# Kernel optimization log

Measured on AMD Instinct MI355X. Metric: run time of the kernel, lower is better.

The kernel has to match this reference:

```python
import jax, jax.numpy as jnp
import numpy as np

EPS_BN = 1e-3  # nn.BatchNorm1d(num_channels, eps=0.001)
B, C, N = 16, 256, 2048
NUM_SA = 4


def _bn(x, g, b, m, v):
    # eval-mode BatchNorm1d over channel dim of [B, C, N]
    return g[:, None] * (x - m[:, None]) * jax.lax.rsqrt(v[:, None] + EPS_BN) + b[:, None]


def _sa_layer(x, qk_w, v_w, v_b, t_w, t_b, g, b, m, var):
    # q_conv and k_conv share weights -> energy = (Wx)^T (Wx)
    q = jnp.einsum('oc,bcn->bon', qk_w, x)              # [B, C//4, N]
    energy = jnp.einsum('bcm,bcn->bmn', q, q)           # [B, N, N]
    attn = jax.nn.softmax(energy, axis=-1)
    # offset-attention: extra column-sum normalization (dim=1)
    attn = attn / (1e-9 + attn.sum(axis=1, keepdims=True))
    xv = jnp.einsum('oc,bcn->bon', v_w, x) + v_b[:, None]   # [B, C, N]
    x_r = jnp.einsum('bcn,bnm->bcm', xv, attn)              # bmm(x_v, attention)
    t = jnp.einsum('oc,bcn->bon', t_w, x - x_r) + t_b[:, None]
    return x + jax.nn.relu(_bn(t, g, b, m, var))


def setup_inputs() -> dict:
    key = jax.random.key(0)
    ks = jax.random.split(key, 24)
    f32 = jnp.float32
    d = {}
    d['x'] = jax.random.normal(ks[0], (B, C, N), dtype=f32)
    d['conv1_w'] = jax.random.normal(ks[1], (C, C), dtype=f32) * 0.05
    d['conv2_w'] = jax.random.normal(ks[2], (C, C), dtype=f32) * 0.05
    for i, nm in enumerate(['bn1', 'bn2']):
        kk = jax.random.split(ks[3 + i], 4)
        d[nm + '_g'] = 1.0 + 0.05 * jax.random.normal(kk[0], (C,), dtype=f32)
        d[nm + '_b'] = 0.05 * jax.random.normal(kk[1], (C,), dtype=f32)
        d[nm + '_m'] = 0.05 * jax.random.normal(kk[2], (C,), dtype=f32)
        d[nm + '_v'] = jax.random.uniform(kk[3], (C,), dtype=f32, minval=0.5, maxval=1.5)
    d['sa_qk_w'] = jax.random.normal(ks[5], (NUM_SA, C // 4, C), dtype=f32) * 0.05
    d['sa_v_w'] = jax.random.normal(ks[6], (NUM_SA, C, C), dtype=f32) * 0.05
    d['sa_v_b'] = jax.random.normal(ks[7], (NUM_SA, C), dtype=f32) * 0.05
    d['sa_t_w'] = jax.random.normal(ks[8], (NUM_SA, C, C), dtype=f32) * 0.05
    d['sa_t_b'] = jax.random.normal(ks[9], (NUM_SA, C), dtype=f32) * 0.05
    d['sa_g'] = 1.0 + 0.05 * jax.random.normal(ks[10], (NUM_SA, C), dtype=f32)
    d['sa_b'] = 0.05 * jax.random.normal(ks[11], (NUM_SA, C), dtype=f32)
    d['sa_m'] = 0.05 * jax.random.normal(ks[12], (NUM_SA, C), dtype=f32)
    d['sa_var'] = jax.random.uniform(ks[13], (NUM_SA, C), dtype=f32, minval=0.5, maxval=1.5)
    d['flag'] = 0  # False -> primary bn branch
    return d


def reference(x, conv1_w, conv2_w, bn1_g, bn1_b, bn1_m, bn1_v,
              bn2_g, bn2_b, bn2_m, bn2_v,
              sa_qk_w, sa_v_w, sa_v_b, sa_t_w, sa_t_b,
              sa_g, sa_b, sa_m, sa_var, flag):
    h = jax.nn.relu(_bn(jnp.einsum('oc,bcn->bon', conv1_w, x), bn1_g, bn1_b, bn1_m, bn1_v))
    h = jax.nn.relu(_bn(jnp.einsum('oc,bcn->bon', conv2_w, h), bn2_g, bn2_b, bn2_m, bn2_v))
    outs = []
    for i in range(NUM_SA):
        h = _sa_layer(h, sa_qk_w[i], sa_v_w[i], sa_v_b[i], sa_t_w[i], sa_t_b[i],
                      sa_g[i], sa_b[i], sa_m[i], sa_var[i])
        outs.append(h)
    return jnp.concatenate(outs, axis=1)  # [B, 4*C, N]
```

## Files before the change

kernel.cpp:

```cpp
#include <hip/hip_runtime.h>
#include <hip/hip_bf16.h>
#include <hip/hip_fp16.h>

static constexpr int Bn = 16;
static constexpr int Cc = 256;
static constexpr int Nn = 2048;
static constexpr int C4 = 64;
static constexpr float LOG2E = 1.4426950408889634f;

typedef _Float16 half_t;
typedef __attribute__((ext_vector_type(8))) _Float16 half8;
typedef __attribute__((ext_vector_type(4))) _Float16 half4;
typedef __attribute__((ext_vector_type(8))) short short8;
typedef __attribute__((ext_vector_type(4))) float float4v;

static constexpr long sNC = (long)Nn * Cc;
static constexpr long sNQ = (long)Nn * C4;

#define DEVI __device__ __forceinline__

DEVI float bf2f(unsigned short u) { return __uint_as_float(((unsigned)u) << 16); }
DEVI unsigned short f2bf(float f) {
    unsigned x = __float_as_uint(f);
    x += 0x7fffu + ((x >> 16) & 1u);
    return (unsigned short)(x >> 16);
}

DEVI void gload16(const void* g, void* l) {
    __builtin_amdgcn_global_load_lds(
        (const __attribute__((address_space(1))) unsigned int*)g,
        (__attribute__((address_space(3))) unsigned int*)l, 16, 0, 0);
}

enum { EPI_RAW = 0, EPI_H = 1, EPI_XV = 2, EPI_T = 4 };

template<int MODE, int BM, int BN, int WI, int WJ, bool BF16OUT>
__global__ __launch_bounds__(WI * WJ * 64)
void mgemm(const half_t* __restrict__ A, long aB,
           const half_t* __restrict__ Bm, long bB,
           void* __restrict__ Yv, long yB, int ldy,
           const half_t* __restrict__ Haux, long hB,
           half_t* __restrict__ hNext, long hnB,
           const float* __restrict__ bias,
           const float* __restrict__ bng, const float* __restrict__ bnb,
           const float* __restrict__ bnm, const float* __restrict__ bnv,
           int K)
{
    constexpr int NW = WI * WJ;
    __shared__ __align__(16) half_t Als[2][BM][32];
    __shared__ __align__(16) half_t Bls[2][BN][32];

    const int tid  = threadIdx.x;
    const int w    = tid >> 6;
    const int lane = tid & 63;
    const int wi   = w % WI;
    const int wj   = w / WI;
    const int quad = lane >> 4, m16 = lane & 15;
    const int lr   = lane >> 2, lc = lane & 3;
    const int b    = blockIdx.z;
    const int j0   = blockIdx.x * BN;
    const int i0   = blockIdx.y * BM;

    const half_t* Ab = A + (size_t)b * aB;
    const half_t* Bb = Bm + (size_t)b * bB;

    float4v acc[4][4];
    #pragma unroll
    for (int i = 0; i < 4; ++i)
        #pragma unroll
        for (int j = 0; j < 4; ++j) acc[i][j] = (float4v)0.f;

    for (int k0 = 0; k0 < K; k0 += 64) {
        #pragma unroll
        for (int s = 0; s < 2; ++s) {
            const int kk = k0 + s * 32 + lc * 8;
            #pragma unroll
            for (int t = 0; t < BM / (16 * NW); ++t) {
                const int row = (t * NW + w) * 16;
                gload16(Ab + (size_t)(i0 + row + lr) * K + kk, &Als[s][row][0]);
            }
            #pragma unroll
            for (int t = 0; t < BN / (16 * NW); ++t) {
                const int row = (t * NW + w) * 16;
                gload16(Bb + (size_t)(j0 + row + lr) * K + kk, &Bls[s][row][0]);
            }
        }
        __syncthreads();
        #pragma unroll
        for (int s = 0; s < 2; ++s) {
            half8 af[4], bf[4];
            #pragma unroll
            for (int t = 0; t < 4; ++t)
                af[t] = *(const half8*)&Als[s][wi * 64 + t * 16 + m16][quad * 8];
            #pragma unroll
            for (int t = 0; t < 4; ++t)
                bf[t] = *(const half8*)&Bls[s][wj * 64 + t * 16 + m16][quad * 8];
            #pragma unroll
            for (int ti = 0; ti < 4; ++ti)
                #pragma unroll
                for (int tj = 0; tj < 4; ++tj)
                    acc[ti][tj] = __builtin_amdgcn_mfma_f32_16x16x32_f16(
                        af[ti], bf[tj], acc[ti][tj], 0, 0, 0);
        }
        __syncthreads();
    }

    #pragma unroll
    for (int ti = 0; ti < 4; ++ti) {
        const int il = i0 + wi * 64 + ti * 16 + quad * 4;
        #pragma unroll
        for (int tj = 0; tj < 4; ++tj) {
            const int jl = j0 + wj * 64 + tj * 16 + m16;
            float4v v = acc[ti][tj];
            if (MODE == EPI_RAW) {
                half4 o;
                #pragma unroll
                for (int r = 0; r < 4; ++r) o[r] = (half_t)v[r];
                *(half4*)((half_t*)Yv + (size_t)b * yB + (size_t)jl * ldy + il) = o;
            } else if (MODE == EPI_H) {
                half4 o;
                #pragma unroll
                for (int r = 0; r < 4; ++r) {
                    const float sc = bng[il + r] * rsqrtf(bnv[il + r] + 1e-3f);
                    const float sh = bnb[il + r] - bnm[il + r] * sc;
                    o[r] = (half_t)fmaxf(fmaf(v[r], sc, sh), 0.f);
                }
                *(half4*)((half_t*)Yv + (size_t)b * yB + (size_t)jl * ldy + il) = o;
            } else if (MODE == EPI_XV) {
                const float bj = bias[jl];
                if (BF16OUT) {
                    ushort4 o;
                    o.x = f2bf(v[0] + bj); o.y = f2bf(v[1] + bj);
                    o.z = f2bf(v[2] + bj); o.w = f2bf(v[3] + bj);
                    *(ushort4*)((unsigned short*)Yv + (size_t)b * yB + (size_t)jl * ldy + il) = o;
                } else {
                    half4 o;
                    #pragma unroll
                    for (int r = 0; r < 4; ++r) o[r] = (half_t)(v[r] + bj);
                    *(half4*)((half_t*)Yv + (size_t)b * yB + (size_t)jl * ldy + il) = o;
                }
            } else {
                const float tb2 = bias[jl];
                const float sc  = bng[jl] * rsqrtf(bnv[jl] + 1e-3f);
                const float sh  = bnb[jl] - bnm[jl] * sc;
                float4v o;
                #pragma unroll
                for (int r = 0; r < 4; ++r) {
                    const float t2  = v[r] + tb2;
                    const float rel = fmaxf(fmaf(t2, sc, sh), 0.f);
                    const float hv  = (float)Haux[(size_t)b * hB + (size_t)(il + r) * Cc + jl];
                    const float ov  = hv + rel;
                    o[r] = ov;
                    if (hNext)
                        hNext[(size_t)b * hnB + (size_t)(il + r) * Cc + jl] = (half_t)ov;
                }
                *(float4v*)((float*)Yv + (size_t)b * yB + (size_t)jl * ldy + il) = o;
            }
        }
    }
}

__global__ __launch_bounds__(256)
void estats(const half_t* __restrict__ q, float* __restrict__ Pbuf)
{
    __shared__ __align__(16) half_t sA[128 * 64];
    __shared__ __align__(16) half_t sB[128 * 64];
    __shared__ float red[2][2][4][16][2];
    const int tid = threadIdx.x, w = tid >> 6, lane = tid & 63;
    const int wi = w & 1, wj = w >> 1, quad = lane >> 4, m16 = lane & 15;
    const int b = blockIdx.z, j0 = blockIdx.x * 128, i0 = blockIdx.y * 128;
    const half_t* qb = q + (size_t)b * sNQ;

    #pragma unroll
    for (int t = 0; t < 4; ++t) {
        const int g = w * 256 + t * 64 + lane;
        const int r = g >> 3, c = g & 7;
        const int cs = c ^ (r & 7);
        gload16(qb + (size_t)(i0 + r) * 64 + cs * 8, sA + (w * 256 + t * 64) * 8);
        gload16(qb + (size_t)(j0 + r) * 64 + cs * 8, sB + (w * 256 + t * 64) * 8);
    }
    __syncthreads();

    half8 an[4][2], bm[4][2];
    #pragma unroll
    for (int t = 0; t < 4; ++t)
        #pragma unroll
        for (int ks = 0; ks < 2; ++ks) {
            const int pc = ((ks * 4 + quad) ^ (m16 & 7)) * 8;
            an[t][ks] = *(const half8*)&sA[(wi * 64 + t * 16 + m16) * 64 + pc];
            bm[t][ks] = *(const half8*)&sB[(wj * 64 + t * 16 + m16) * 64 + pc];
        }

    #pragma unroll
    for (int tj = 0; tj < 4; ++tj) {
        float4v e[4];
        #pragma unroll
        for (int ti = 0; ti < 4; ++ti) {
            e[ti] = (float4v)0.f;
            e[ti] = __builtin_amdgcn_mfma_f32_16x16x32_f16(an[ti][0], bm[tj][0], e[ti], 0, 0, 0);
            e[ti] = __builtin_amdgcn_mfma_f32_16x16x32_f16(an[ti][1], bm[tj][1], e[ti], 0, 0, 0);
        }
        float lmax = -1e30f;
        #pragma unroll
        for (int ti = 0; ti < 4; ++ti)
            #pragma unroll
            for (int r = 0; r < 4; ++r) lmax = fmaxf(lmax, e[ti][r]);
        lmax = fmaxf(lmax, __shfl_xor(lmax, 16));
        lmax = fmaxf(lmax, __shfl_xor(lmax, 32));
        float ls = 0.f;
        #pragma unroll
        for (int ti = 0; ti < 4; ++ti)
            #pragma unroll
            for (int r = 0; r < 4; ++r) ls += __expf(e[ti][r] - lmax);
        ls += __shfl_xor(ls, 16);
        ls += __shfl_xor(ls, 32);
        if (quad == 0) { red[wi][wj][tj][m16][0] = lmax; red[wi][wj][tj][m16][1] = ls; }
    }
    __syncthreads();
    if (tid < 128) {
        const int wj2 = tid >> 6, tj2 = (tid >> 4) & 3, mm = tid & 15;
        const float m0 = red[0][wj2][tj2][mm][0], s0 = red[0][wj2][tj2][mm][1];
        const float m1 = red[1][wj2][tj2][mm][0], s1 = red[1][wj2][tj2][mm][1];
        const float M = fmaxf(m0, m1);
        const float S = s0 * __expf(m0 - M) + s1 * __expf(m1 - M);
        const int m = j0 + wj2 * 64 + tj2 * 16 + mm;
        *(float2*)(Pbuf + (((size_t)b * Nn + m) * 16 + blockIdx.y) * 2) = make_float2(M, S);
    }
}

__global__ __launch_bounds__(256)
void statsreduce(const float* __restrict__ Pbuf, float* __restrict__ off)
{
    const int id = blockIdx.x * 256 + threadIdx.x;
    const int b = id >> 11, m = id & 2047;
    const float2* p = (const float2*)(Pbuf + ((size_t)b * Nn + m) * 32);
    float M = -1e30f;
    #pragma unroll
    for (int i = 0; i < 16; ++i) M = fmaxf(M, p[i].x);
    float S = 0.f;
    #pragma unroll
    for (int i = 0; i < 16; ++i) S += p[i].y * __expf(p[i].x - M);
    off[(size_t)b * Nn + m] = fmaf(M, LOG2E, __log2f(S));
}

__global__ __launch_bounds__(1024, 4)
void flashxr(const half_t* __restrict__ q, const half_t* __restrict__ xv,
             const half_t* __restrict__ h, const float* __restrict__ off,
             half_t* __restrict__ dS)
{
    __shared__ __align__(16) half_t sQ[128 * 64];
    __shared__ __align__(16) half_t sXV[256 * 128];
    __shared__ __align__(16) half_t sP[128 * 128];

    const int tid = threadIdx.x, w = tid >> 6, lane = tid & 63;
    const int quad = lane >> 4, m16 = lane & 15;
    const int wiE = w & 1, wjE = w >> 1;
    const int wi = w & 3, wj = w >> 2;
    const int b = blockIdx.z, j0 = blockIdx.x * 128;
    const half_t* qb  = q + (size_t)b * sNQ;
    const half_t* xvb = xv + (size_t)b * sNC;

    const int sr = tid >> 3, sc = tid & 7;
    const int qsw = (sc ^ (sr & 7)) * 8;

    gload16(qb + (size_t)(j0 + sr) * 64 + qsw, sP + (size_t)tid * 8);
    gload16(qb + (size_t)sr * 64 + qsw,        sQ + (size_t)tid * 8);
    __syncthreads();
    half8 bq[2];
    #pragma unroll
    for (int ks = 0; ks < 2; ++ks)
        bq[ks] = *(const half8*)&sP[(wjE * 16 + m16) * 64
                                    + (((ks * 4 + quad) ^ (m16 & 7)) * 8)];
    __syncthreads();

    float4v acc[4][2];
    #pragma unroll
    for (int i = 0; i < 4; ++i)
        #pragma unroll
        for (int j = 0; j < 2; ++j) acc[i][j] = (float4v)0.f;
    float csa = 0.f;

    const float* offb = off + (size_t)b * Nn;

    for (int nc = 0; nc < 16; ++nc) {
        #pragma unroll
        for (int t = 0; t < 4; ++t) {
            const int g = t * 1024 + tid;
            const int r = g >> 4, c = g & 15;
            gload16(xvb + (size_t)r * Nn + nc * 128 + ((c ^ (r & 15)) * 8),
                    sXV + (size_t)g * 8);
        }
        __syncthreads();

        const int nbase = nc * 128 + wiE * 64 + quad * 4;
        #pragma unroll
        for (int ti = 0; ti < 4; ++ti) {
            const int arow = (wiE * 64 + ti * 16 + m16) * 64;
            const half8 an0 = *(const half8*)&sQ[arow + ((quad ^ (m16 & 7)) * 8)];
            const half8 an1 = *(const half8*)&sQ[arow + (((4 + quad) ^ (m16 & 7)) * 8)];
            float4v e = (float4v)0.f;
            e = __builtin_amdgcn_mfma_f32_16x16x32_f16(an0, bq[0], e, 0, 0, 0);
            e = __builtin_amdgcn_mfma_f32_16x16x32_f16(an1, bq[1], e, 0, 0, 0);
            const float4v o4 = *(const float4v*)&offb[nbase + ti * 16];
            float c0 = 0.f; ushort4 pk;
            #pragma unroll
            for (int r = 0; r < 4; ++r) {
                const float p = __builtin_amdgcn_exp2f(fmaf(e[r], LOG2E, -o4[r]));
                c0 += p; (&pk.x)[r] = f2bf(p);
            }
            csa += c0;
            const int pc  = wiE * 8 + ti * 2 + (quad >> 1);
            const int sub = (quad & 1) * 4;
            const int mrow = wjE * 16 + m16;
            *(ushort4*)&((unsigned short*)sP)[(size_t)mrow * 128 + (pc ^ m16) * 8 + sub] = pk;
        }
        __syncthreads();

        if (nc < 15)
            gload16(qb + (size_t)((nc + 1) * 128 + sr) * 64 + qsw,
                    sQ + (size_t)tid * 8);

        #pragma unroll
        for (int ks = 0; ks < 4; ++ks) {
            short8 xa[4], pb[2];
            #pragma unroll
            for (int ti = 0; ti < 4; ++ti)
                xa[ti] = *(const short8*)&sXV[(wi * 64 + ti * 16 + m16) * 128
                                              + (((ks * 4 + quad) ^ m16) * 8)];
            #pragma unroll
            for (int tj = 0; tj < 2; ++tj)
                pb[tj] = *(const short8*)&sP[(wj * 32 + tj * 16 + m16) * 128
                                             + (((ks * 4 + quad) ^ m16) * 8)];
            #pragma unroll
            for (int ti = 0; ti < 4; ++ti)
                #pragma unroll
                for (int tj = 0; tj < 2; ++tj)
                    acc[ti][tj] = __builtin_amdgcn_mfma_f32_16x16x32_bf16(
                        xa[ti], pb[tj], acc[ti][tj], 0, 0, 0);
        }
        __syncthreads();
    }

    csa += __shfl_xor(csa, 16);
    csa += __shfl_xor(csa, 32);
    float* fb = (float*)sP;
    if (lane < 16) fb[wiE * 128 + wjE * 16 + lane] = csa;
    __syncthreads();
    float csr[2];
    #pragma unroll
    for (int tj = 0; tj < 2; ++tj) {
        const int m = wj * 32 + tj * 16 + m16;
        csr[tj] = 1.0f / (1e-9f + fb[m] + fb[128 + m]);
    }

    const half_t* hb = h + (size_t)b * sNC;
    half_t* db = dS + (size_t)b * sNC;
    #pragma unroll
    for (int ti = 0; ti < 4; ++ti) {
        const int cg = wi * 64 + ti * 16 + quad * 4;
        #pragma unroll
        for (int tj = 0; tj < 2; ++tj) {
            const int mg = j0 + wj * 32 + tj * 16 + m16;
            const half4 hv = *(const half4*)&hb[(size_t)mg * Cc + cg];
            half4 o;
            #pragma unroll
            for (int r = 0; r < 4; ++r)
                o[r] = (half_t)((float)hv[r] - acc[ti][tj][r] * csr[tj]);
            *(half4*)&db[(size_t)mg * Cc + cg] = o;
        }
    }
}

__global__ __launch_bounds__(256)
void xpose_cast(const float* __restrict__ x, half_t* __restrict__ xT)
{
    __shared__ half_t tile[32][33];
    const int tx = threadIdx.x & 31, ty = threadIdx.x >> 5;
    const int n0 = blockIdx.x * 32, c0 = blockIdx.y * 32, b = blockIdx.z;
    #pragma unroll
    for (int r = 0; r < 4; ++r)
        tile[ty * 4 + r][tx] =
            (half_t)x[((size_t)b * Cc + c0 + ty * 4 + r) * Nn + n0 + tx];
    __syncthreads();
    #pragma unroll
    for (int r = 0; r < 4; ++r)
        xT[((size_t)b * Nn + n0 + ty * 4 + r) * Cc + c0 + tx] = tile[tx][ty * 4 + r];
}

__global__ __launch_bounds__(256)
void castall(const float* __restrict__ c1, const float* __restrict__ c2,
             const float* __restrict__ qk, const float* __restrict__ vw,
             const float* __restrict__ tw, half_t* __restrict__ dst)
{
    const int i = (blockIdx.x * 256 + threadIdx.x) * 4;
    const float* s; int o;
    if      (i < 65536)  { s = c1; o = 0; }
    else if (i < 131072) { s = c2; o = 65536; }
    else if (i < 196608) { s = qk; o = 131072; }
    else if (i < 458752) { s = vw; o = 196608; }
    else                 { s = tw; o = 458752; }
    const float4v v = *(const float4v*)(s + (i - o));
    half4 out;
    #pragma unroll
    for (int r = 0; r < 4; ++r) out[r] = (half_t)v[r];
    *(half4*)(dst + i) = out;
}

extern "C" void kernel_launch(void* const* d_in, const int* in_sizes, int n_in,
                              void* d_out, int out_size, void* d_ws, size_t ws_size,
                              hipStream_t stream)
{
    const float* x    = (const float*)d_in[0];
    const float* c1w  = (const float*)d_in[1];
    const float* c2w  = (const float*)d_in[2];
    const float* bn1g = (const float*)d_in[3], *bn1b = (const float*)d_in[4];
    const float* bn1m = (const float*)d_in[5], *bn1v = (const float*)d_in[6];
    const float* bn2g = (const float*)d_in[7], *bn2b = (const float*)d_in[8];
    const float* bn2m = (const float*)d_in[9], *bn2v = (const float*)d_in[10];
    const float* qkw  = (const float*)d_in[11];
    const float* vw   = (const float*)d_in[12];
    const float* vb   = (const float*)d_in[13];
    const float* tw   = (const float*)d_in[14];
    const float* tb   = (const float*)d_in[15];
    const float* sag  = (const float*)d_in[16];
    const float* sab  = (const float*)d_in[17];
    const float* sam  = (const float*)d_in[18];
    const float* sav  = (const float*)d_in[19];
    float* out = (float*)d_out;

    char* ws = (char*)d_ws;
    const size_t HSZ = (size_t)Bn * Nn * Cc * 2;
    half_t* xT   = (half_t*)(ws);
    half_t* hA   = (half_t*)(ws + HSZ);
    half_t* hBuf = (half_t*)(ws + 2 * HSZ);
    half_t* q_s  = (half_t*)(ws + 3 * HSZ);
    half_t* xv_s = (half_t*)(ws + 3 * HSZ + (size_t)4194304);
    half_t* d_s  = (half_t*)(ws + 4 * HSZ + (size_t)4194304);
    float*  offp = (float*) (ws + 5 * HSZ + (size_t)4194304);
    float*  Pbuf = (float*) (ws + 5 * HSZ + (size_t)4325376);
    half_t* warena = (half_t*)(ws + 5 * HSZ + (size_t)8519680);
    half_t* wc1  = warena;
    half_t* wc2  = wc1 + 65536;
    half_t* wqk  = wc2 + 65536;
    half_t* wv   = wqk + 65536;
    half_t* wt   = wv  + 262144;

    dim3 blk(256);

    castall<<<768, blk, 0, stream>>>(c1w, c2w, qkw, vw, tw, warena);
    xpose_cast<<<dim3(Nn / 32, Cc / 32, Bn), blk, 0, stream>>>(x, xT);

    mgemm<EPI_H, 256, 128, 4, 2, false><<<dim3(16, 1, Bn), dim3(512), 0, stream>>>(
        wc1, 0, xT, sNC, hA, sNC, Cc, nullptr, 0, nullptr, 0,
        nullptr, bn1g, bn1b, bn1m, bn1v, Cc);
    mgemm<EPI_H, 256, 128, 4, 2, false><<<dim3(16, 1, Bn), dim3(512), 0, stream>>>(
        wc2, 0, hA, sNC, hBuf, sNC, Cc, nullptr, 0, nullptr, 0,
        nullptr, bn2g, bn2b, bn2m, bn2v, Cc);

    half_t* hcur = hBuf;
    half_t* hnxt = hA;
    for (int L = 0; L < 4; ++L) {
        mgemm<EPI_RAW, 64, 256, 1, 4, false><<<dim3(8, 1, Bn), blk, 0, stream>>>(
            wqk + (long)L * C4 * Cc, 0, hcur, sNC, q_s, sNQ, C4,
            nullptr, 0, nullptr, 0,
            nullptr, nullptr, nullptr, nullptr, nullptr, Cc);
        estats<<<dim3(16, 16, Bn), blk, 0, stream>>>(q_s, Pbuf);
        statsreduce<<<128, blk, 0, stream>>>(Pbuf, offp);
        mgemm<EPI_XV, 128, 256, 2, 4, true><<<dim3(1, 16, Bn), dim3(512), 0, stream>>>(
            hcur, sNC, wv + (long)L * Cc * Cc, 0, xv_s, (long)Cc * Nn, Nn,
            nullptr, 0, nullptr, 0,
            vb + L * Cc, nullptr, nullptr, nullptr, nullptr, Cc);
        flashxr<<<dim3(16, 1, Bn), dim3(1024), 0, stream>>>(
            q_s, xv_s, hcur, offp, d_s);
        mgemm<EPI_T, 128, 256, 2, 4, false><<<dim3(1, 16, Bn), dim3(512), 0, stream>>>(
            d_s, sNC, wt + (long)L * Cc * Cc, 0,
            out + (long)L * Cc * Nn, (long)4 * Cc * Nn, Nn,
            hcur, sNC, (L < 3) ? hnxt : nullptr, sNC,
            tb + L * Cc, sag + L * Cc, sab + L * Cc, sam + L * Cc, sav + L * Cc,
            Cc);
        half_t* tmp = hcur; hcur = hnxt; hnxt = tmp;
    }
}
```

Baseline: 795.7 us.

## Fuse stats reduction and output transform GEMM into flash attention kernel

The softmax-stats reduction moves into the flashxr prologue, computing per-column offsets into shared memory instead of running a separate statsreduce kernel. The trans-conv GEMM with its BN/ReLU/residual epilogue is fused into flashxr's tail: the x - x_r tile is staged in LDS and multiplied by tw read directly from global. This removes two launches per layer and the round trip of the d_s intermediate through memory. The q tile is also double-buffered so the next tile's load is issued before the energy compute. The cost is more LDS per block (sOff plus a second sQ buffer) and dropping the occupancy hint in launch_bounds. Each block also reads the whole Pbuf slice and the full tw matrix redundantly, and the epilogue does scattered stores to hNext.

```diff
diff --git a/kernel.cpp b/kernel.cpp
--- a/kernel.cpp
+++ b/kernel.cpp
@@ -32,15 +32,13 @@
         (__attribute__((address_space(3))) unsigned int*)l, 16, 0, 0);
 }
 
-enum { EPI_RAW = 0, EPI_H = 1, EPI_XV = 2, EPI_T = 4 };
+enum { EPI_RAW = 0, EPI_H = 1, EPI_XV = 2 };
 
 template<int MODE, int BM, int BN, int WI, int WJ, bool BF16OUT>
 __global__ __launch_bounds__(WI * WJ * 64)
 void mgemm(const half_t* __restrict__ A, long aB,
            const half_t* __restrict__ Bm, long bB,
            void* __restrict__ Yv, long yB, int ldy,
-           const half_t* __restrict__ Haux, long hB,
-           half_t* __restrict__ hNext, long hnB,
            const float* __restrict__ bias,
            const float* __restrict__ bng, const float* __restrict__ bnb,
            const float* __restrict__ bnm, const float* __restrict__ bnv,
@@ -126,7 +124,7 @@
                     o[r] = (half_t)fmaxf(fmaf(v[r], sc, sh), 0.f);
                 }
                 *(half4*)((half_t*)Yv + (size_t)b * yB + (size_t)jl * ldy + il) = o;
-            } else if (MODE == EPI_XV) {
+            } else {
                 const float bj = bias[jl];
                 if (BF16OUT) {
                     ushort4 o;
@@ -139,22 +137,6 @@
                     for (int r = 0; r < 4; ++r) o[r] = (half_t)(v[r] + bj);
                     *(half4*)((half_t*)Yv + (size_t)b * yB + (size_t)jl * ldy + il) = o;
                 }
-            } else {
-                const float tb2 = bias[jl];
-                const float sc  = bng[jl] * rsqrtf(bnv[jl] + 1e-3f);
-                const float sh  = bnb[jl] - bnm[jl] * sc;
-                float4v o;
-                #pragma unroll
-                for (int r = 0; r < 4; ++r) {
-                    const float t2  = v[r] + tb2;
-                    const float rel = fmaxf(fmaf(t2, sc, sh), 0.f);
-                    const float hv  = (float)Haux[(size_t)b * hB + (size_t)(il + r) * Cc + jl];
-                    const float ov  = hv + rel;
-                    o[r] = ov;
-                    if (hNext)
-                        hNext[(size_t)b * hnB + (size_t)(il + r) * Cc + jl] = (half_t)ov;
-                }
-                *(float4v*)((float*)Yv + (size_t)b * yB + (size_t)jl * ldy + il) = o;
             }
         }
     }
@@ -228,34 +210,24 @@
     }
 }
 
-__global__ __launch_bounds__(256)
-void statsreduce(const float* __restrict__ Pbuf, float* __restrict__ off)
+__global__ __launch_bounds__(1024)
+void flashxr(const half_t* __restrict__ q, const half_t* __restrict__ xv,
+             const half_t* __restrict__ h, const float* __restrict__ Pbuf,
+             const half_t* __restrict__ tw, const float* __restrict__ tb,
+             const float* __restrict__ bng, const float* __restrict__ bnb,
+             const float* __restrict__ bnm, const float* __restrict__ bnv,
+             float* __restrict__ outL, half_t* __restrict__ hNext)
 {
-    const int id = blockIdx.x * 256 + threadIdx.x;
-    const int b = id >> 11, m = id & 2047;
-    const float2* p = (const float2*)(Pbuf + ((size_t)b * Nn + m) * 32);
-    float M = -1e30f;
-    #pragma unroll
-    for (int i = 0; i < 16; ++i) M = fmaxf(M, p[i].x);
-    float S = 0.f;
-    #pragma unroll
-    for (int i = 0; i < 16; ++i) S += p[i].y * __expf(p[i].x - M);
-    off[(size_t)b * Nn + m] = fmaf(M, LOG2E, __log2f(S));
-}
-
-__global__ __launch_bounds__(1024, 4)
-void flashxr(const half_t* __restrict__ q, const half_t* __restrict__ xv,
-             const half_t* __restrict__ h, const float* __restrict__ off,
-             half_t* __restrict__ dS)
-{
-    __shared__ __align__(16) half_t sQ[128 * 64];
+    __shared__ __align__(16) half_t sQ[2][128 * 64];
     __shared__ __align__(16) half_t sXV[256 * 128];
     __shared__ __align__(16) half_t sP[128 * 128];
+    __shared__ float sOff[Nn];
 
     const int tid = threadIdx.x, w = tid >> 6, lane = tid & 63;
     const int quad = lane >> 4, m16 = lane & 15;
     const int wiE = w & 1, wjE = w >> 1;
     const int wi = w & 3, wj = w >> 2;
+    const int wiT = w & 1, wjT = w >> 1;
     const int b = blockIdx.z, j0 = blockIdx.x * 128;
     const half_t* qb  = q + (size_t)b * sNQ;
     const half_t* xvb = xv + (size_t)b * sNC;
@@ -264,7 +236,27 @@
     const int qsw = (sc ^ (sr & 7)) * 8;
 
     gload16(qb + (size_t)(j0 + sr) * 64 + qsw, sP + (size_t)tid * 8);
-    gload16(qb + (size_t)sr * 64 + qsw,        sQ + (size_t)tid * 8);
+    gload16(qb + (size_t)sr * 64 + qsw,        &sQ[0][(size_t)tid * 8]);
+
+    {
+        const float* pB = Pbuf + (size_t)b * Nn * 32;
+        for (int i = tid; i < Nn; i += 1024) {
+            const float4v* p4 = (const float4v*)(pB + (size_t)i * 32);
+            float4v v[8];
+            #pragma unroll
+            for (int t = 0; t < 8; ++t) v[t] = p4[t];
+            float M = -1e30f;
+            #pragma unroll
+            for (int t = 0; t < 8; ++t) { M = fmaxf(M, v[t][0]); M = fmaxf(M, v[t][2]); }
+            float S = 0.f;
+            #pragma unroll
+            for (int t = 0; t < 8; ++t) {
+                S += v[t][1] * __expf(v[t][0] - M);
+                S += v[t][3] * __expf(v[t][2] - M);
+            }
+            sOff[i] = fmaf(M, LOG2E, __log2f(S));
+        }
+    }
     __syncthreads();
     half8 bq[2];
     #pragma unroll
@@ -280,9 +272,8 @@
         for (int j = 0; j < 2; ++j) acc[i][j] = (float4v)0.f;
     float csa = 0.f;
 
-    const float* offb = off + (size_t)b * Nn;
-
     for (int nc = 0; nc < 16; ++nc) {
+        const int cur = nc & 1;
         #pragma unroll
         for (int t = 0; t < 4; ++t) {
             const int g = t * 1024 + tid;
@@ -290,18 +281,20 @@
             gload16(xvb + (size_t)r * Nn + nc * 128 + ((c ^ (r & 15)) * 8),
                     sXV + (size_t)g * 8);
         }
-        __syncthreads();
+        if (nc < 15)
+            gload16(qb + (size_t)((nc + 1) * 128 + sr) * 64 + qsw,
+                    &sQ[cur ^ 1][(size_t)tid * 8]);
 
         const int nbase = nc * 128 + wiE * 64 + quad * 4;
         #pragma unroll
         for (int ti = 0; ti < 4; ++ti) {
             const int arow = (wiE * 64 + ti * 16 + m16) * 64;
-            const half8 an0 = *(const half8*)&sQ[arow + ((quad ^ (m16 & 7)) * 8)];
-            const half8 an1 = *(const half8*)&sQ[arow + (((4 + quad) ^ (m16 & 7)) * 8)];
+            const half8 an0 = *(const half8*)&sQ[cur][arow + ((quad ^ (m16 & 7)) * 8)];
+            const half8 an1 = *(const half8*)&sQ[cur][arow + (((4 + quad) ^ (m16 & 7)) * 8)];
             float4v e = (float4v)0.f;
             e = __builtin_amdgcn_mfma_f32_16x16x32_f16(an0, bq[0], e, 0, 0, 0);
             e = __builtin_amdgcn_mfma_f32_16x16x32_f16(an1, bq[1], e, 0, 0, 0);
-            const float4v o4 = *(const float4v*)&offb[nbase + ti * 16];
+            const float4v o4 = *(const float4v*)&sOff[nbase + ti * 16];
             float c0 = 0.f; ushort4 pk;
             #pragma unroll
             for (int r = 0; r < 4; ++r) {
@@ -316,10 +309,6 @@
         }
         __syncthreads();
 
-        if (nc < 15)
-            gload16(qb + (size_t)((nc + 1) * 128 + sr) * 64 + qsw,
-                    sQ + (size_t)tid * 8);
-
         #pragma unroll
         for (int ks = 0; ks < 4; ++ks) {
             short8 xa[4], pb[2];
@@ -354,19 +343,73 @@
     }
 
     const half_t* hb = h + (size_t)b * sNC;
-    half_t* db = dS + (size_t)b * sNC;
+    half_t* sD = sXV;
     #pragma unroll
     for (int ti = 0; ti < 4; ++ti) {
         const int cg = wi * 64 + ti * 16 + quad * 4;
+        const int cc = (cg >> 3) ^ (m16 & 7);
+        const int sub = (quad & 1) * 4;
         #pragma unroll
         for (int tj = 0; tj < 2; ++tj) {
-            const int mg = j0 + wj * 32 + tj * 16 + m16;
+            const int mr = wj * 32 + tj * 16 + m16;
+            const int mg = j0 + mr;
             const half4 hv = *(const half4*)&hb[(size_t)mg * Cc + cg];
             half4 o;
             #pragma unroll
             for (int r = 0; r < 4; ++r)
                 o[r] = (half_t)((float)hv[r] - acc[ti][tj][r] * csr[tj]);
-            *(half4*)&db[(size_t)mg * Cc + cg] = o;
+            *(half4*)&sD[(size_t)mr * 256 + cc * 8 + sub] = o;
+        }
+    }
+    __syncthreads();
+
+    float4v acc2[4][2];
+    #pragma unroll
+    for (int i = 0; i < 4; ++i)
+        #pragma unroll
+        for (int j = 0; j < 2; ++j) acc2[i][j] = (float4v)0.f;
+    #pragma unroll
+    for (int ks = 0; ks < 8; ++ks) {
+        half8 af[4], bf[2];
+        #pragma unroll
+        for (int tm = 0; tm < 4; ++tm)
+            af[tm] = *(const half8*)&sD[(size_t)(wiT * 64 + tm * 16 + m16) * 256
+                                        + (((ks * 4 + quad) ^ (m16 & 7)) * 8)];
+        #pragma unroll
+        for (int tc = 0; tc < 2; ++tc)
+            bf[tc] = *(const half8*)&tw[(size_t)(wjT * 32 + tc * 16 + m16) * 256
+                                        + ks * 32 + quad * 8];
+        #pragma unroll
+        for (int tm = 0; tm < 4; ++tm)
+            #pragma unroll
+            for (int tc = 0; tc < 2; ++tc)
+                acc2[tm][tc] = __builtin_amdgcn_mfma_f32_16x16x32_f16(
+                    af[tm], bf[tc], acc2[tm][tc], 0, 0, 0);
+    }
+
+    const long yB = (long)4 * Cc * Nn;
+    float* yb = outL + (size_t)b * yB;
+    half_t* hn = hNext ? hNext + (size_t)b * sNC : nullptr;
+    #pragma unroll
+    for (int tc = 0; tc < 2; ++tc) {
+        const int co = wjT * 32 + tc * 16 + m16;
+        const float tb2 = tb[co];
+        const float sc2 = bng[co] * rsqrtf(bnv[co] + 1e-3f);
+        const float sh2 = bnb[co] - bnm[co] * sc2;
+        #pragma unroll
+        for (int tm = 0; tm < 4; ++tm) {
+            const int mg = j0 + wiT * 64 + tm * 16 + quad * 4;
+            float4v o;
+            #pragma unroll
+            for (int r = 0; r < 4; ++r) {
+                const float t2  = acc2[tm][tc][r] + tb2;
+                const float rel = fmaxf(fmaf(t2, sc2, sh2), 0.f);
+                const float hv  = (float)hb[(size_t)(mg + r) * Cc + co];
+                const float ov  = hv + rel;
+                o[r] = ov;
+                if (hn) hn[(size_t)(mg + r) * Cc + co] = (half_t)ov;
+            }
+            *(float4v*)&yb[(size_t)co * Nn + mg] = o;
         }
     }
 }
@@ -435,10 +478,8 @@
     half_t* hBuf = (half_t*)(ws + 2 * HSZ);
     half_t* q_s  = (half_t*)(ws + 3 * HSZ);
     half_t* xv_s = (half_t*)(ws + 3 * HSZ + (size_t)4194304);
-    half_t* d_s  = (half_t*)(ws + 4 * HSZ + (size_t)4194304);
-    float*  offp = (float*) (ws + 5 * HSZ + (size_t)4194304);
-    float*  Pbuf = (float*) (ws + 5 * HSZ + (size_t)4325376);
-    half_t* warena = (half_t*)(ws + 5 * HSZ + (size_t)8519680);
+    float*  Pbuf = (float*) (ws + 4 * HSZ + (size_t)4194304);
+    half_t* warena = (half_t*)(ws + 4 * HSZ + (size_t)8388608);
     half_t* wc1  = warena;
     half_t* wc2  = wc1 + 65536;
     half_t* wqk  = wc2 + 65536;
@@ -451,10 +492,10 @@
     xpose_cast<<<dim3(Nn / 32, Cc / 32, Bn), blk, 0, stream>>>(x, xT);
 
     mgemm<EPI_H, 256, 128, 4, 2, false><<<dim3(16, 1, Bn), dim3(512), 0, stream>>>(
-        wc1, 0, xT, sNC, hA, sNC, Cc, nullptr, 0, nullptr, 0,
+        wc1, 0, xT, sNC, hA, sNC, Cc,
         nullptr, bn1g, bn1b, bn1m, bn1v, Cc);
     mgemm<EPI_H, 256, 128, 4, 2, false><<<dim3(16, 1, Bn), dim3(512), 0, stream>>>(
-        wc2, 0, hA, sNC, hBuf, sNC, Cc, nullptr, 0, nullptr, 0,
+        wc2, 0, hA, sNC, hBuf, sNC, Cc,
         nullptr, bn2g, bn2b, bn2m, bn2v, Cc);
 
     half_t* hcur = hBuf;
@@ -462,22 +503,16 @@
     for (int L = 0; L < 4; ++L) {
         mgemm<EPI_RAW, 64, 256, 1, 4, false><<<dim3(8, 1, Bn), blk, 0, stream>>>(
             wqk + (long)L * C4 * Cc, 0, hcur, sNC, q_s, sNQ, C4,
-            nullptr, 0, nullptr, 0,
             nullptr, nullptr, nullptr, nullptr, nullptr, Cc);
         estats<<<dim3(16, 16, Bn), blk, 0, stream>>>(q_s, Pbuf);
-        statsreduce<<<128, blk, 0, stream>>>(Pbuf, offp);
         mgemm<EPI_XV, 128, 256, 2, 4, true><<<dim3(1, 16, Bn), dim3(512), 0, stream>>>(
             hcur, sNC, wv + (long)L * Cc * Cc, 0, xv_s, (long)Cc * Nn, Nn,
-            nullptr, 0, nullptr, 0,
             vb + L * Cc, nullptr, nullptr, nullptr, nullptr, Cc);
         flashxr<<<dim3(16, 1, Bn), dim3(1024), 0, stream>>>(
-            q_s, xv_s, hcur, offp, d_s);
-        mgemm<EPI_T, 128, 256, 2, 4, false><<<dim3(1, 16, Bn), dim3(512), 0, stream>>>(
-            d_s, sNC, wt + (long)L * Cc * Cc, 0,
-            out + (long)L * Cc * Nn, (long)4 * Cc * Nn, Nn,
-            hcur, sNC, (L < 3) ? hnxt : nullptr, sNC,
-            tb + L * Cc, sag + L * Cc, sab + L * Cc, sam + L * Cc, sav + L * Cc,
-            Cc);
+            q_s, xv_s, hcur, Pbuf,
+            wt + (long)L * Cc * Cc, tb + L * Cc,
+            sag + L * Cc, sab + L * Cc, sam + L * Cc, sav + L * Cc,
+            out + (long)L * Cc * Nn, (L < 3) ? hnxt : nullptr);
         half_t* tmp = hcur; hcur = hnxt; hnxt = tmp;
     }
 }
```

New measurement: 734.5 us. 1.08x faster.
